# Kernel optimization log

Measured on AMD Instinct MI355X. Metric: run time of the kernel, lower is better.

## Reference

```python
import jax, jax.numpy as jnp
import numpy as np

REG_MAX = 16
NC = 80
NO = 4 * REG_MAX + NC  # 144
STRIDES = (8, 16, 32)


def _make_anchors(shapes, strides, offset=0.5):
    # shapes: list of (h, w). Returns anchors [2, A], stride_row [1, A]
    pts, sts = [], []
    for (h, w), s in zip(shapes, strides):
        sx = jnp.arange(w, dtype=jnp.float32) + offset
        sy = jnp.arange(h, dtype=jnp.float32) + offset
        gy, gx = jnp.meshgrid(sy, sx, indexing='ij')
        pts.append(jnp.stack([gx, gy], -1).reshape(-1, 2))
        sts.append(jnp.full((h * w,), float(s), dtype=jnp.float32))
    anchors = jnp.concatenate(pts, 0).T            # [2, A]
    stride_row = jnp.concatenate(sts, 0)[None, :]  # [1, A]
    return anchors, stride_row


def setup_inputs() -> dict:
    key = jax.random.key(0)
    k0, k1, k2 = jax.random.split(key, 3)
    b = 64
    return {
        'feat0': jax.random.normal(k0, (b, NO, 80, 80), dtype=jnp.float32),
        'feat1': jax.random.normal(k1, (b, NO, 40, 40), dtype=jnp.float32),
        'feat2': jax.random.normal(k2, (b, NO, 20, 20), dtype=jnp.float32),
    }


def reference(feat0, feat1, feat2):
    feats = [feat0, feat1, feat2]
    b = feat0.shape[0]
    shapes = [(f.shape[2], f.shape[3]) for f in feats]
    anchors, stride_row = _make_anchors(shapes, STRIDES, 0.5)

    # flatten spatial dims and concat over levels: y [b, no, A]
    y = jnp.concatenate([f.reshape(b, NO, -1) for f in feats], axis=2)
    box_logits = y[:, : 4 * REG_MAX]                # [b, 64, A]
    scores = jax.nn.sigmoid(y[:, 4 * REG_MAX:])     # [b, nc, A]

    # DFL decode: softmax over reg_max bins, expectation via arange
    d = box_logits.reshape(b, 4, REG_MAX, -1).transpose(0, 1, 3, 2)  # [b,4,A,reg_max]
    proj = jnp.arange(REG_MAX, dtype=d.dtype)
    dist = jnp.einsum('bfar,r->bfa', jax.nn.softmax(d, axis=-1), proj)  # [b,4,A]

    lt = -dist[:, :2]   # left/top offsets (negated)
    rb = dist[:, 2:]    # right/bottom offsets
    # anchors tiled to [b, 4, A]; boxes in (x1, y1, x2, y2) * stride
    boxes = (jnp.tile(anchors[None], (b, 2, 1)) + jnp.concatenate([lt, rb], axis=1)) * stride_row

    # NMS in the source is a TRT plugin stub; faithful math ends here.
    return boxes.transpose(0, 2, 1), scores.transpose(0, 2, 1)  # [b,A,4], [b,A,nc]
```

## Files before the change

kernel.cpp:

```cpp
#include <hip/hip_runtime.h>
#include <math.h>

#define NO_CH   144
#define NC      80
#define REGMAX  16
#define A_TOT   8400
#define HW0     6400
#define HW1     1600
#define HW2     400
#define SC_BLOCKS 132

typedef float f32x4 __attribute__((ext_vector_type(4)));

__device__ __forceinline__ float rcpf(float x) { return __builtin_amdgcn_rcpf(x); }
__device__ __forceinline__ float sigmoidf(float x) {
    return rcpf(1.0f + __expf(-x));
}

__global__ __launch_bounds__(256, 6) void fused_kernel(
    const float* __restrict__ f0, const float* __restrict__ f1,
    const float* __restrict__ f2, float* __restrict__ out_boxes,
    float* __restrict__ out_scores)
{
    __shared__ float tile[NC][65];
    __shared__ float dist_lds[4][64];

    const int b   = blockIdx.y;
    const int a0  = blockIdx.x * 64;
    const int tid = threadIdx.x;

    const float* base; int hw, local; float st;
    if (a0 < HW0) {
        base = f0 + (size_t)b * NO_CH * HW0; hw = HW0; local = a0; st = 8.0f;
    } else if (a0 < HW0 + HW1) {
        base = f1 + (size_t)b * NO_CH * HW1; hw = HW1; local = a0 - HW0; st = 16.0f;
    } else {
        base = f2 + (size_t)b * NO_CH * HW2; hw = HW2; local = a0 - HW0 - HW1; st = 32.0f;
    }

    const int nvalid = min(64, A_TOT - a0);

    {
        const int g    = tid >> 6;
        const int lane = tid & 63;
        const int laq  = lane & 15;
        const int rq   = lane >> 4;

        float4 se = make_float4(0.f, 0.f, 0.f, 0.f);
        float4 sw = make_float4(0.f, 0.f, 0.f, 0.f);

        if (laq * 4 < nvalid) {
            const float* s = base + (size_t)(g * REGMAX + rq * 4) * hw + local + laq * 4;
            #pragma unroll
            for (int r = 0; r < 4; ++r) {
                const float4 v = *reinterpret_cast<const float4*>(s + (size_t)r * hw);
                const float wgt = (float)(rq * 4 + r);
                const float ex = __expf(v.x);
                const float ey = __expf(v.y);
                const float ez = __expf(v.z);
                const float ew = __expf(v.w);
                se.x += ex; se.y += ey; se.z += ez; se.w += ew;
                sw.x += ex * wgt; sw.y += ey * wgt; sw.z += ez * wgt; sw.w += ew * wgt;
            }
        }
        #pragma unroll
        for (int m = 16; m <= 32; m <<= 1) {
            se.x += __shfl_xor(se.x, m, 64);
            se.y += __shfl_xor(se.y, m, 64);
            se.z += __shfl_xor(se.z, m, 64);
            se.w += __shfl_xor(se.w, m, 64);
            sw.x += __shfl_xor(sw.x, m, 64);
            sw.y += __shfl_xor(sw.y, m, 64);
            sw.z += __shfl_xor(sw.z, m, 64);
            sw.w += __shfl_xor(sw.w, m, 64);
        }
        if (rq == 0 && laq * 4 < nvalid) {
            const float4 dist = make_float4(sw.x * rcpf(se.x), sw.y * rcpf(se.y),
                                            sw.z * rcpf(se.z), sw.w * rcpf(se.w));
            *reinterpret_cast<float4*>(&dist_lds[g][laq * 4]) = dist;
        }
    }

    const float* ssc = base + (size_t)(4 * REGMAX) * hw + local;
    if (nvalid == 64) {
        const int quad = tid & 15;
        const int r0   = tid >> 4;
        #pragma unroll
        for (int i = 0; i < 5; ++i) {
            const int r = r0 + 16 * i;
            const float4 v = *reinterpret_cast<const float4*>(
                ssc + (size_t)r * hw + quad * 4);
            tile[r][quad * 4 + 0] = sigmoidf(v.x);
            tile[r][quad * 4 + 1] = sigmoidf(v.y);
            tile[r][quad * 4 + 2] = sigmoidf(v.z);
            tile[r][quad * 4 + 3] = sigmoidf(v.w);
        }
    } else {
        const int col = tid & 63;
        const int r0  = tid >> 6;
        if (col < nvalid) {
            #pragma unroll
            for (int i = 0; i < 20; ++i) {
                const int r = r0 + 4 * i;
                tile[r][col] = sigmoidf(ssc[(size_t)r * hw + col]);
            }
        }
    }

    __syncthreads();

    if (tid < 4 * nvalid) {
        const int la   = tid >> 2;
        const int comp = tid & 3;
        const int gl   = local + la;
        int ix, iy;
        if (hw == HW0)      { iy = gl / 80; ix = gl - iy * 80; }
        else if (hw == HW1) { iy = gl / 40; ix = gl - iy * 40; }
        else                { iy = gl / 20; ix = gl - iy * 20; }
        const float axy = ((comp & 1) ? (float)iy : (float)ix) + 0.5f;
        const float d   = dist_lds[comp][la];
        const float val = (axy + ((comp >= 2) ? d : -d)) * st;
        __builtin_nontemporal_store(
            val, out_boxes + ((size_t)b * A_TOT + a0) * 4 + tid);
    }

    float* dst = out_scores + ((size_t)b * A_TOT + a0) * NC;
    const int nq = nvalid * (NC / 4);
    for (int j4 = tid; j4 < nq; j4 += 256) {
        const int la = j4 / 20;
        const int c0 = (j4 - la * 20) * 4;
        f32x4 o;
        o.x = tile[c0 + 0][la];
        o.y = tile[c0 + 1][la];
        o.z = tile[c0 + 2][la];
        o.w = tile[c0 + 3][la];
        __builtin_nontemporal_store(o, reinterpret_cast<f32x4*>(dst) + j4);
    }
}

extern "C" void kernel_launch(void* const* d_in, const int* in_sizes, int n_in,
                              void* d_out, int out_size, void* d_ws, size_t ws_size,
                              hipStream_t stream) {
    const float* f0 = (const float*)d_in[0];
    const float* f1 = (const float*)d_in[1];
    const float* f2 = (const float*)d_in[2];

    const int b = in_sizes[0] / (NO_CH * HW0);

    float* out_boxes  = (float*)d_out;
    float* out_scores = out_boxes + (size_t)b * A_TOT * 4;

    dim3 grid(SC_BLOCKS, b);
    fused_kernel<<<grid, dim3(256), 0, stream>>>(f0, f1, f2, out_boxes, out_scores);
}
```

Baseline: 84.63 us.

## Process 128 anchors per block with per-level tiling

Doubles the anchors handled per block from 64 to 128 and tiles each pyramid level separately, so no tile crosses a level boundary. The grid shrinks from 132 to 67 blocks per batch, and each thread does more loads, exp work and stores. Rows are 512 bytes per channel instead of 256, which may improve coalescing and cut per-block overhead. LDS use roughly doubles and launch_bounds drops to 3 blocks per CU, which lowers occupancy.

```diff
diff --git a/kernel.cpp b/kernel.cpp
--- a/kernel.cpp
+++ b/kernel.cpp
@@ -8,7 +8,11 @@
 #define HW0     6400
 #define HW1     1600
 #define HW2     400
-#define SC_BLOCKS 132
+
+#define T0      50
+#define T1      13
+#define T2      4
+#define NTILES  (T0 + T1 + T2)
 
 typedef float f32x4 __attribute__((ext_vector_type(4)));
 
@@ -17,44 +21,51 @@
     return rcpf(1.0f + __expf(-x));
 }
 
-__global__ __launch_bounds__(256, 6) void fused_kernel(
+__global__ __launch_bounds__(256, 3) void fused_kernel(
     const float* __restrict__ f0, const float* __restrict__ f1,
     const float* __restrict__ f2, float* __restrict__ out_boxes,
     float* __restrict__ out_scores)
 {
-    __shared__ float tile[NC][65];
-    __shared__ float dist_lds[4][64];
+    __shared__ float tile[NC][129];
+    __shared__ float dist_lds[4][128];
 
-    const int b   = blockIdx.y;
-    const int a0  = blockIdx.x * 64;
-    const int tid = threadIdx.x;
+    const int b    = blockIdx.y;
+    const int t    = blockIdx.x;
+    const int tid  = threadIdx.x;
+    const int lane = tid & 63;
+    const int wv   = tid >> 6;
 
-    const float* base; int hw, local; float st;
-    if (a0 < HW0) {
-        base = f0 + (size_t)b * NO_CH * HW0; hw = HW0; local = a0; st = 8.0f;
-    } else if (a0 < HW0 + HW1) {
-        base = f1 + (size_t)b * NO_CH * HW1; hw = HW1; local = a0 - HW0; st = 16.0f;
+    const float* base; int hw, local, w, nvalid; float st; int a0;
+    if (t < T0) {
+        base = f0 + (size_t)b * NO_CH * HW0; hw = HW0; local = t * 128;
+        w = 80; st = 8.0f;  nvalid = 128;               a0 = local;
+    } else if (t < T0 + T1) {
+        base = f1 + (size_t)b * NO_CH * HW1; hw = HW1; local = (t - T0) * 128;
+        w = 40; st = 16.0f; nvalid = min(128, HW1 - local); a0 = HW0 + local;
     } else {
-        base = f2 + (size_t)b * NO_CH * HW2; hw = HW2; local = a0 - HW0 - HW1; st = 32.0f;
+        base = f2 + (size_t)b * NO_CH * HW2; hw = HW2; local = (t - T0 - T1) * 128;
+        w = 20; st = 32.0f; nvalid = min(128, HW2 - local); a0 = HW0 + HW1 + local;
     }
 
-    const int nvalid = min(64, A_TOT - a0);
-
     {
-        const int g    = tid >> 6;
-        const int lane = tid & 63;
-        const int laq  = lane & 15;
-        const int rq   = lane >> 4;
+        const int g  = wv;
+        const int rq = lane >> 5;
+        const int q  = lane & 31;
+        const bool act = (q * 4 < nvalid);
 
         float4 se = make_float4(0.f, 0.f, 0.f, 0.f);
         float4 sw = make_float4(0.f, 0.f, 0.f, 0.f);
 
-        if (laq * 4 < nvalid) {
-            const float* s = base + (size_t)(g * REGMAX + rq * 4) * hw + local + laq * 4;
+        #pragma unroll
+        for (int i = 0; i < 2; ++i) {
             #pragma unroll
             for (int r = 0; r < 4; ++r) {
-                const float4 v = *reinterpret_cast<const float4*>(s + (size_t)r * hw);
-                const float wgt = (float)(rq * 4 + r);
+                const int ch = rq * 4 + r + 8 * i;
+                float4 v = make_float4(0.f, 0.f, 0.f, 0.f);
+                if (act)
+                    v = *reinterpret_cast<const float4*>(
+                        base + (size_t)(g * REGMAX + ch) * hw + local + q * 4);
+                const float wgt = (float)ch;
                 const float ex = __expf(v.x);
                 const float ey = __expf(v.y);
                 const float ez = __expf(v.z);
@@ -63,65 +74,59 @@
                 sw.x += ex * wgt; sw.y += ey * wgt; sw.z += ez * wgt; sw.w += ew * wgt;
             }
         }
-        #pragma unroll
-        for (int m = 16; m <= 32; m <<= 1) {
-            se.x += __shfl_xor(se.x, m, 64);
-            se.y += __shfl_xor(se.y, m, 64);
-            se.z += __shfl_xor(se.z, m, 64);
-            se.w += __shfl_xor(se.w, m, 64);
-            sw.x += __shfl_xor(sw.x, m, 64);
-            sw.y += __shfl_xor(sw.y, m, 64);
-            sw.z += __shfl_xor(sw.z, m, 64);
-            sw.w += __shfl_xor(sw.w, m, 64);
-        }
-        if (rq == 0 && laq * 4 < nvalid) {
+        se.x += __shfl_xor(se.x, 32, 64);
+        se.y += __shfl_xor(se.y, 32, 64);
+        se.z += __shfl_xor(se.z, 32, 64);
+        se.w += __shfl_xor(se.w, 32, 64);
+        sw.x += __shfl_xor(sw.x, 32, 64);
+        sw.y += __shfl_xor(sw.y, 32, 64);
+        sw.z += __shfl_xor(sw.z, 32, 64);
+        sw.w += __shfl_xor(sw.w, 32, 64);
+
+        if (rq == 0 && act) {
             const float4 dist = make_float4(sw.x * rcpf(se.x), sw.y * rcpf(se.y),
                                             sw.z * rcpf(se.z), sw.w * rcpf(se.w));
-            *reinterpret_cast<float4*>(&dist_lds[g][laq * 4]) = dist;
+            *reinterpret_cast<float4*>(&dist_lds[g][q * 4]) = dist;
         }
     }
 
-    const float* ssc = base + (size_t)(4 * REGMAX) * hw + local;
-    if (nvalid == 64) {
-        const int quad = tid & 15;
-        const int r0   = tid >> 4;
+    {
+        const float* ssc = base + (size_t)(4 * REGMAX) * hw + local;
+        const int q    = lane & 31;
+        const int rsub = lane >> 5;
+        const bool act = (q * 4 < nvalid);
         #pragma unroll
-        for (int i = 0; i < 5; ++i) {
-            const int r = r0 + 16 * i;
-            const float4 v = *reinterpret_cast<const float4*>(
-                ssc + (size_t)r * hw + quad * 4);
-            tile[r][quad * 4 + 0] = sigmoidf(v.x);
-            tile[r][quad * 4 + 1] = sigmoidf(v.y);
-            tile[r][quad * 4 + 2] = sigmoidf(v.z);
-            tile[r][quad * 4 + 3] = sigmoidf(v.w);
-        }
-    } else {
-        const int col = tid & 63;
-        const int r0  = tid >> 6;
-        if (col < nvalid) {
-            #pragma unroll
-            for (int i = 0; i < 20; ++i) {
-                const int r = r0 + 4 * i;
-                tile[r][col] = sigmoidf(ssc[(size_t)r * hw + col]);
-            }
+        for (int i = 0; i < 10; ++i) {
+            const int r = wv * 20 + rsub + 2 * i;
+            float4 u = make_float4(0.f, 0.f, 0.f, 0.f);
+            if (act)
+                u = *reinterpret_cast<const float4*>(ssc + (size_t)r * hw + q * 4);
+            tile[r][q * 4 + 0] = sigmoidf(u.x);
+            tile[r][q * 4 + 1] = sigmoidf(u.y);
+            tile[r][q * 4 + 2] = sigmoidf(u.z);
+            tile[r][q * 4 + 3] = sigmoidf(u.w);
         }
     }
 
     __syncthreads();
 
-    if (tid < 4 * nvalid) {
-        const int la   = tid >> 2;
-        const int comp = tid & 3;
-        const int gl   = local + la;
-        int ix, iy;
-        if (hw == HW0)      { iy = gl / 80; ix = gl - iy * 80; }
-        else if (hw == HW1) { iy = gl / 40; ix = gl - iy * 40; }
-        else                { iy = gl / 20; ix = gl - iy * 20; }
-        const float axy = ((comp & 1) ? (float)iy : (float)ix) + 0.5f;
-        const float d   = dist_lds[comp][la];
-        const float val = (axy + ((comp >= 2) ? d : -d)) * st;
-        __builtin_nontemporal_store(
-            val, out_boxes + ((size_t)b * A_TOT + a0) * 4 + tid);
+    #pragma unroll
+    for (int p = 0; p < 2; ++p) {
+        const int idx = tid + 256 * p;
+        if (idx < 4 * nvalid) {
+            const int la   = idx >> 2;
+            const int comp = idx & 3;
+            const int gl   = local + la;
+            int iy, ix;
+            if (w == 80)      { iy = gl / 80; ix = gl - iy * 80; }
+            else if (w == 40) { iy = gl / 40; ix = gl - iy * 40; }
+            else              { iy = gl / 20; ix = gl - iy * 20; }
+            const float axy = ((comp & 1) ? (float)iy : (float)ix) + 0.5f;
+            const float d   = dist_lds[comp][la];
+            const float val = (axy + ((comp >= 2) ? d : -d)) * st;
+            __builtin_nontemporal_store(
+                val, out_boxes + ((size_t)b * A_TOT + a0) * 4 + idx);
+        }
     }
 
     float* dst = out_scores + ((size_t)b * A_TOT + a0) * NC;
@@ -150,6 +155,6 @@
     float* out_boxes  = (float*)d_out;
     float* out_scores = out_boxes + (size_t)b * A_TOT * 4;
 
-    dim3 grid(SC_BLOCKS, b);
+    dim3 grid(NTILES, b);
     fused_kernel<<<grid, dim3(256), 0, stream>>>(f0, f1, f2, out_boxes, out_scores);
 }
```

Result: slower. 111.1 us (+31.3%).
